# Performance work log

Measured on AMD Instinct MI355X. Metric: run time of the kernel, lower is better.

The kernel has to match this reference:

```python
import jax, jax.numpy as jnp
import numpy as np

N_NODES = 100000


def _gcn_layer(x, W, b, src, dst, ew):
    # support = x @ W  (dense transform first, standard GCN)
    support = x @ W  # [N, out]
    # sparse propagate: out[i] = sum_{e: dst[e]=i} ew[e] * support[src[e]]
    msgs = support[src] * ew[:, None]  # [E, out]
    out = jax.ops.segment_sum(msgs, dst, num_segments=N_NODES)
    return out + b


def setup_inputs() -> dict:
    key = jax.random.key(0)
    ks = jax.random.split(key, 7)
    nfeat, nhid, nclass, E = 512, 256, 40, 3200000
    x = jax.random.normal(ks[0], (N_NODES, nfeat), dtype=jnp.float32)
    edge_index = jax.random.randint(ks[1], (2, E), 0, N_NODES, dtype=jnp.int32)
    edge_weight = jax.random.uniform(ks[2], (E,), dtype=jnp.float32)
    W1 = jax.random.normal(ks[3], (nfeat, nhid), dtype=jnp.float32) / np.sqrt(nfeat)
    b1 = jnp.zeros((nhid,), dtype=jnp.float32)
    W2 = jax.random.normal(ks[4], (nhid, nclass), dtype=jnp.float32) / np.sqrt(nhid)
    b2 = jnp.zeros((nclass,), dtype=jnp.float32)
    return {"x": x, "edge_index": edge_index, "edge_weight": edge_weight,
            "W1": W1, "b1": b1, "W2": W2, "b2": b2}


def reference(x, edge_index, edge_weight, W1, b1, W2, b2):
    src, dst = edge_index[0], edge_index[1]
    h = _gcn_layer(x, W1, b1, src, dst, edge_weight)
    h = jax.nn.relu(h)  # with_relu=True; dropout skipped (eval mode)
    h = _gcn_layer(h, W2, b2, src, dst, edge_weight)
    return jax.nn.log_softmax(h, axis=1)
```

## Files before the change

kernel.cpp:

```cpp
#include <hip/hip_runtime.h>
#include <math.h>

#define N_NODES 100000
#define M_PAD 100096
#define NFEAT 512
#define NHID 256
#define NCLASS 40
#define SUP2_LD 48

#define NBKT 250
#define NPB 400
#define BINA_CHUNK 3072
#define BCAP 14336

#define GEMM1_TILES 782
#define GEMM1_BLOCKS 391

typedef __attribute__((ext_vector_type(8))) short bf16x8;
typedef __attribute__((ext_vector_type(4))) float f32x4;

__device__ __forceinline__ unsigned short f2bf(float f) {
    unsigned int u = __builtin_bit_cast(unsigned int, f);
    u += 0x7fffu + ((u >> 16) & 1u);
    return (unsigned short)(u >> 16);
}
__device__ __forceinline__ void bf2x2(unsigned int u, float& f0, float& f1) {
    f0 = __builtin_bit_cast(float, u << 16);
    f1 = __builtin_bit_cast(float, u & 0xffff0000u);
}
__device__ __forceinline__ void gload16(const void* g, void* l) {
    __builtin_amdgcn_global_load_lds(
        (const __attribute__((address_space(1))) unsigned int*)g,
        (__attribute__((address_space(3))) unsigned int*)l, 16, 0, 0);
}
template <int CODE>
__device__ __forceinline__ float swzx(float v) {
    return __builtin_bit_cast(float,
        __builtin_amdgcn_ds_swizzle(__builtin_bit_cast(int, v), CODE));
}

#define CVTW_BLOCKS 512

__global__ __launch_bounds__(256) void k_init(int* __restrict__ bcur,
                                              const float* __restrict__ W1,
                                              unsigned short* __restrict__ w1t,
                                              const float* __restrict__ W2,
                                              uint4* __restrict__ w2f) {
    int b = blockIdx.x;
    int t = threadIdx.x;
    if (b == 0) {
        if (t < NBKT) bcur[t] = t * BCAP;
    } else if (b <= CVTW_BLOCKS) {
        int idx = (b - 1) * 256 + t;
        int n = idx >> 9, k = idx & 511;
        w1t[idx] = f2bf(W1[(size_t)k * NHID + n]);
    } else {
        for (int idx = t; idx < 8 * 3 * 64; idx += 256) {
            int ks = idx / 192;
            int rem = idx - ks * 192;
            int n = rem >> 6;
            int l = rem & 63;
            int col = n * 16 + (l & 15);
            int kbase = ks * 32 + (l >> 4) * 8;
            unsigned short o[8];
#pragma unroll
            for (int j = 0; j < 8; ++j)
                o[j] = (col < NCLASS) ? f2bf(W2[(size_t)(kbase + j) * NCLASS + col]) : 0;
            w2f[idx] = *(const uint4*)o;
        }
    }
}

__device__ __forceinline__ void binA_body(char* smbase, int t, int cblk,
                                          const int* __restrict__ src,
                                          const int* __restrict__ dst,
                                          const float* __restrict__ ew,
                                          int* __restrict__ bcur,
                                          uint2* __restrict__ tmp, int E) {
    uint2* sorted = (uint2*)smbase;
    unsigned char* bkt8 = (unsigned char*)(smbase + 24576);
    int* cnt = (int*)(smbase + 27648);
    int* startv = cnt + 256;
    int* offv = startv + 256;
    int* gb = offv + 256;
    int c0 = cblk * BINA_CHUNK;
    int n = min(BINA_CHUNK, E - c0);
    cnt[t] = 0;
    __syncthreads();
    for (int j = t; j < n; j += 256) {
        atomicAdd(&cnt[(unsigned)dst[c0 + j] / NPB], 1);
    }
    __syncthreads();
    int v = cnt[t];
    startv[t] = v;
    __syncthreads();
    for (int o = 1; o < 256; o <<= 1) {
        int a = (t >= o) ? startv[t - o] : 0;
        __syncthreads();
        startv[t] += a;
        __syncthreads();
    }
    int ex = startv[t] - v;
    __syncthreads();
    startv[t] = ex;
    offv[t] = ex;
    if (t < NBKT) gb[t] = (v > 0) ? atomicAdd(&bcur[t], v) : 0;
    __syncthreads();
    for (int j = t; j < n; j += 256) {
        int d = dst[c0 + j];
        int b = (unsigned)d / NPB;
        int dl = d - b * NPB;
        int r = atomicAdd(&offv[b], 1);
        sorted[r] = make_uint2((unsigned)src[c0 + j] | ((unsigned)dl << 17),
                               __builtin_bit_cast(unsigned, ew[c0 + j]));
        bkt8[r] = (unsigned char)b;
    }
    __syncthreads();
    for (int j = t; j < n; j += 256) {
        int b = bkt8[j];
        tmp[gb[b] + (j - startv[b])] = sorted[j];
    }
}

__device__ __forceinline__ void gemm1_body(char* smem, int t, int mb,
                                           const float* __restrict__ x,
                                           const unsigned short* __restrict__ w1t,
                                           unsigned short* __restrict__ sup1) {
    const int w = t >> 6, lane = t & 63;
    const int m0 = mb * 128;
    const int wm = w >> 1, wn = w & 1;
    const int r15 = lane & 15, hi = lane >> 4;

    f32x4 acc[4][8];
#pragma unroll
    for (int i = 0; i < 4; ++i)
#pragma unroll
        for (int j = 0; j < 8; ++j) acc[i][j] = (f32x4){0.f, 0.f, 0.f, 0.f};

    const char* wsrc = (const char*)w1t;

#define STAGE1(kt, b)                                                                  \
    {                                                                                  \
        char* Ab = smem + (b) * 8192;                                                  \
        char* Bb = smem + 16384 + (b) * 16384;                                         \
        _Pragma("unroll") for (int i = 0; i < 2; ++i) {                                \
            int u = i * 256 + t;                                                       \
            int row = u >> 2, part = u & 3;                                            \
            int gr = m0 + row;                                                         \
            unsigned short ob[8];                                                      \
            if (gr < N_NODES) {                                                        \
                const float* sp = x + (size_t)gr * NFEAT + (kt) * 32 + part * 8;       \
                float4 v0 = *(const float4*)sp;                                        \
                float4 v1 = *(const float4*)(sp + 4);                                  \
                ob[0] = f2bf(v0.x); ob[1] = f2bf(v0.y);                                \
                ob[2] = f2bf(v0.z); ob[3] = f2bf(v0.w);                                \
                ob[4] = f2bf(v1.x); ob[5] = f2bf(v1.y);                                \
                ob[6] = f2bf(v1.z); ob[7] = f2bf(v1.w);                                \
            } else {                                                                   \
                _Pragma("unroll") for (int j = 0; j < 8; ++j) ob[j] = 0;               \
            }                                                                          \
            *(uint4*)(Ab + row * 64 + ((part ^ ((row >> 1) & 3)) << 4)) =              \
                *(const uint4*)ob;                                                     \
        }                                                                              \
        _Pragma("unroll") for (int i = 0; i < 4; ++i) {                                \
            int u = i * 256 + t;                                                       \
            int nrow = u >> 2, part = u & 3;                                           \
            int q = part ^ ((nrow >> 1) & 3);                                          \
            gload16(wsrc + (size_t)nrow * 1024 + (kt) * 64 + q * 16, Bb + u * 16);     \
        }                                                                              \
    }

    STAGE1(0, 0);
    for (int kt = 0; kt < 16; ++kt) {
        __syncthreads();
        if (kt < 15) STAGE1(kt + 1, (kt + 1) & 1);
        const char* Ab = smem + (kt & 1) * 8192;
        const char* Bb = smem + 16384 + (kt & 1) * 16384;
        bf16x8 a[4], bb[8];
#pragma unroll
        for (int i = 0; i < 4; ++i) {
            int r = wm * 64 + i * 16 + r15;
            a[i] = *(const bf16x8*)(Ab + r * 64 + ((hi ^ ((r >> 1) & 3)) << 4));
        }
#pragma unroll
        for (int j = 0; j < 8; ++j) {
            int n = wn * 128 + j * 16 + r15;
            bb[j] = *(const bf16x8*)(Bb + n * 64 + ((hi ^ ((n >> 1) & 3)) << 4));
        }
#pragma unroll
        for (int i = 0; i < 4; ++i)
#pragma unroll
            for (int j = 0; j < 8; ++j)
                acc[i][j] = __builtin_amdgcn_mfma_f32_16x16x32_bf16(a[i], bb[j], acc[i][j], 0, 0, 0);
    }
#undef STAGE1

#pragma unroll
    for (int i = 0; i < 4; ++i) {
        int rowb = m0 + wm * 64 + i * 16 + hi * 4;
#pragma unroll
        for (int j = 0; j < 8; ++j) {
            int col = wn * 128 + j * 16 + r15;
#pragma unroll
            for (int r = 0; r < 4; ++r)
                sup1[(size_t)(rowb + r) * NHID + col] = f2bf(acc[i][j][r]);
        }
    }
}

__global__ __launch_bounds__(256) void k_fat(const float* __restrict__ x,
                                             const unsigned short* __restrict__ w1t,
                                             unsigned short* __restrict__ sup1,
                                             const int* __restrict__ src,
                                             const int* __restrict__ dst,
                                             const float* __restrict__ ew,
                                             int* __restrict__ bcur,
                                             uint2* __restrict__ tmp, int E) {
    __shared__ __align__(16) char smem[49152];
    int b = blockIdx.x;
    int t = threadIdx.x;
    if (b < GEMM1_BLOCKS) {
        gemm1_body(smem, t, b, x, w1t, sup1);
        __syncthreads();
        gemm1_body(smem, t, b + GEMM1_BLOCKS, x, w1t, sup1);
    } else {
        binA_body(smem, t, b - GEMM1_BLOCKS, src, dst, ew, bcur, tmp, E);
    }
}

__global__ __launch_bounds__(256) void k_binB(const uint2* __restrict__ tmp,
                                              const int* __restrict__ bcur,
                                              int* __restrict__ rowptr,
                                              uint2* __restrict__ cedge) {
    __shared__ int sc[256];
    __shared__ int nc[NPB];
    __shared__ int st[NPB];
    int b = blockIdx.x, t = threadIdx.x;
    int c = (t < NBKT) ? (bcur[t] - t * BCAP) : 0;
    sc[t] = c;
    __syncthreads();
    for (int o = 1; o < 256; o <<= 1) {
        int a = (t >= o) ? sc[t - o] : 0;
        __syncthreads();
        sc[t] += a;
        __syncthreads();
    }
    int base = (b == 0) ? 0 : sc[b - 1];
    int mycnt = sc[b] - base;
    int total = sc[NBKT - 1];
    __syncthreads();
    for (int i = t; i < NPB; i += 256) nc[i] = 0;
    __syncthreads();
    const uint2* srcp = tmp + (size_t)b * BCAP;
    for (int j = t; j < mycnt; j += 256) atomicAdd(&nc[srcp[j].x >> 17], 1);
    __syncthreads();
    int v0 = nc[t];
    sc[t] = v0;
    __syncthreads();
    for (int o = 1; o < 256; o <<= 1) {
        int a = (t >= o) ? sc[t - o] : 0;
        __syncthreads();
        sc[t] += a;
        __syncthreads();
    }
    int tot0 = sc[255];
    st[t] = sc[t] - v0;
    __syncthreads();
    int v1 = (t < NPB - 256) ? nc[256 + t] : 0;
    sc[t] = v1;
    __syncthreads();
    for (int o = 1; o < 256; o <<= 1) {
        int a = (t >= o) ? sc[t - o] : 0;
        __syncthreads();
        sc[t] += a;
        __syncthreads();
    }
    if (t < NPB - 256) st[256 + t] = tot0 + sc[t] - v1;
    __syncthreads();
    int n0 = b * NPB;
    for (int i = t; i < NPB; i += 256) {
        int s = base + st[i];
        rowptr[n0 + i] = s;
        st[i] = s;
    }
    if (b == NBKT - 1 && t == 0) rowptr[N_NODES] = total;
    __syncthreads();
    for (int j = t; j < mycnt; j += 256) {
        uint2 e = srcp[j];
        int dl = e.x >> 17;
        int addr = atomicAdd(&st[dl], 1);
        cedge[addr] = make_uint2(e.x & 0x1FFFFu, e.y);
    }
}

__global__ __launch_bounds__(256) void k_prop1(const unsigned short* __restrict__ sup1,
                                               const int* __restrict__ rowptr,
                                               const uint2* __restrict__ cedge,
                                               const float* __restrict__ b1,
                                               unsigned short* __restrict__ h1) {
    int gid = blockIdx.x * blockDim.x + threadIdx.x;
    int wid = gid >> 6;
    int lane = gid & 63;
    if (wid >= N_NODES) return;
    int beg = rowptr[wid], end = rowptr[wid + 1];
    float a0 = 0.f, a1 = 0.f, a2 = 0.f, a3 = 0.f;
    int e = beg;
    for (; e + 7 < end; e += 8) {
        uint2 ed[8];
#pragma unroll
        for (int q = 0; q < 8; ++q) ed[q] = cedge[e + q];
        uint2 r[8];
#pragma unroll
        for (int q = 0; q < 8; ++q)
            r[q] = *(const uint2*)(sup1 + (size_t)ed[q].x * NHID + lane * 4);
#pragma unroll
        for (int q = 0; q < 8; ++q) {
            float wq = __builtin_bit_cast(float, ed[q].y);
            float f0, f1, f2, f3;
            bf2x2(r[q].x, f0, f1);
            bf2x2(r[q].y, f2, f3);
            a0 += wq * f0; a1 += wq * f1; a2 += wq * f2; a3 += wq * f3;
        }
    }
    for (; e < end; ++e) {
        uint2 ed = cedge[e];
        float wq = __builtin_bit_cast(float, ed.y);
        uint2 rv = *(const uint2*)(sup1 + (size_t)ed.x * NHID + lane * 4);
        float f0, f1, f2, f3;
        bf2x2(rv.x, f0, f1);
        bf2x2(rv.y, f2, f3);
        a0 += wq * f0; a1 += wq * f1; a2 += wq * f2; a3 += wq * f3;
    }
    float4 bv = *(const float4*)(b1 + lane * 4);
    a0 = fmaxf(a0 + bv.x, 0.f);
    a1 = fmaxf(a1 + bv.y, 0.f);
    a2 = fmaxf(a2 + bv.z, 0.f);
    a3 = fmaxf(a3 + bv.w, 0.f);
    unsigned short o[4] = {f2bf(a0), f2bf(a1), f2bf(a2), f2bf(a3)};
    *(uint2*)(h1 + (size_t)wid * NHID + lane * 4) = *(const uint2*)o;
}

__global__ __launch_bounds__(256) void k_gemm2(const unsigned short* __restrict__ h1,
                                               const uint4* __restrict__ w2f,
                                               unsigned short* __restrict__ sup2) {
    int t = threadIdx.x;
    int w = t >> 6, lane = t & 63;
    int m0 = (blockIdx.x * 4 + w) * 16;
    int r15 = lane & 15, hi = lane >> 4;

    bf16x8 bfrag[8][3];
#pragma unroll
    for (int ks = 0; ks < 8; ++ks)
#pragma unroll
        for (int n = 0; n < 3; ++n)
            bfrag[ks][n] = __builtin_bit_cast(bf16x8, w2f[(ks * 3 + n) * 64 + lane]);

    f32x4 acc[3];
#pragma unroll
    for (int n = 0; n < 3; ++n) acc[n] = (f32x4){0.f, 0.f, 0.f, 0.f};

    const unsigned short* arow = h1 + (size_t)(m0 + r15) * NHID + hi * 8;
#pragma unroll
    for (int ks = 0; ks < 8; ++ks) {
        bf16x8 a = *(const bf16x8*)(arow + ks * 32);
#pragma unroll
        for (int n = 0; n < 3; ++n)
            acc[n] = __builtin_amdgcn_mfma_f32_16x16x32_bf16(a, bfrag[ks][n], acc[n], 0, 0, 0);
    }
#pragma unroll
    for (int n = 0; n < 3; ++n) {
        int col = n * 16 + r15;
#pragma unroll
        for (int r = 0; r < 4; ++r) {
            int row = m0 + hi * 4 + r;
            sup2[(size_t)row * SUP2_LD + col] = f2bf(acc[n][r]);
        }
    }
}

__global__ __launch_bounds__(256) void k_prop2(const unsigned short* __restrict__ sup2,
                                               const int* __restrict__ rowptr,
                                               const uint2* __restrict__ cedge,
                                               const float* __restrict__ b2,
                                               float* __restrict__ out) {
    int gid = blockIdx.x * blockDim.x + threadIdx.x;
    int wv = gid >> 6;
    int lane = gid & 63;
    int grp = lane >> 4;
    int gl = lane & 15;
    int wid = wv * 4 + grp;
    if (wid >= N_NODES) return;
    int beg = rowptr[wid], end = rowptr[wid + 1];
    bool act = gl < 10;
    int c4 = gl * 4;
    float acc0 = 0.f, acc1 = 0.f, acc2 = 0.f, acc3 = 0.f;
    int e = beg;
    for (; e + 7 < end; e += 8) {
        uint2 ed[8];
#pragma unroll
        for (int q = 0; q < 8; ++q) ed[q] = cedge[e + q];
        uint2 u[8];
#pragma unroll
        for (int q = 0; q < 8; ++q)
            u[q] = act ? *(const uint2*)(sup2 + (size_t)ed[q].x * SUP2_LD + c4)
                       : make_uint2(0u, 0u);
#pragma unroll
        for (int q = 0; q < 8; ++q) {
            float wq = __builtin_bit_cast(float, ed[q].y);
            float f0, f1, f2, f3;
            bf2x2(u[q].x, f0, f1);
            bf2x2(u[q].y, f2, f3);
            acc0 += wq * f0; acc1 += wq * f1; acc2 += wq * f2; acc3 += wq * f3;
        }
    }
    for (; e < end; ++e) {
        uint2 eq = cedge[e];
        uint2 u = act ? *(const uint2*)(sup2 + (size_t)eq.x * SUP2_LD + c4)
                      : make_uint2(0u, 0u);
        float wq = __builtin_bit_cast(float, eq.y);
        float f0, f1, f2, f3;
        bf2x2(u.x, f0, f1);
        bf2x2(u.y, f2, f3);
        acc0 += wq * f0; acc1 += wq * f1; acc2 += wq * f2; acc3 += wq * f3;
    }
    float v0 = -INFINITY, v1 = -INFINITY, v2 = -INFINITY, v3 = -INFINITY;
    if (act) {
        float4 bb = *(const float4*)(b2 + c4);
        v0 = acc0 + bb.x;
        v1 = acc1 + bb.y;
        v2 = acc2 + bb.z;
        v3 = acc3 + bb.w;
    }
    float m = fmaxf(fmaxf(v0, v1), fmaxf(v2, v3));
    m = fmaxf(m, swzx<0x201F>(m));
    m = fmaxf(m, swzx<0x101F>(m));
    m = fmaxf(m, swzx<0x081F>(m));
    m = fmaxf(m, swzx<0x041F>(m));
    float s = act ? (expf(v0 - m) + expf(v1 - m) + expf(v2 - m) + expf(v3 - m)) : 0.f;
    s += swzx<0x201F>(s);
    s += swzx<0x101F>(s);
    s += swzx<0x081F>(s);
    s += swzx<0x041F>(s);
    if (act) {
        float ls = logf(s);
        float4 o = make_float4(v0 - m - ls, v1 - m - ls, v2 - m - ls, v3 - m - ls);
        *(float4*)(out + (size_t)wid * NCLASS + c4) = o;
    }
}


extern "C" void kernel_launch(void* const* d_in, const int* in_sizes, int n_in,
                              void* d_out, int out_size, void* d_ws, size_t ws_size,
                              hipStream_t stream) {
    const float* x = (const float*)d_in[0];
    const int* ei = (const int*)d_in[1];
    const float* ew = (const float*)d_in[2];
    const float* W1 = (const float*)d_in[3];
    const float* b1 = (const float*)d_in[4];
    const float* W2 = (const float*)d_in[5];
    const float* b2 = (const float*)d_in[6];
    float* out = (float*)d_out;

    int E = in_sizes[1] / 2;
    const int* src = ei;
    const int* dst = ei + E;

    char* w = (char*)d_ws;
    size_t off = 0;
    auto alloc = [&](size_t bytes) {
        void* p = w + off;
        off += (bytes + 255) & ~(size_t)255;
        return p;
    };
    unsigned short* w1t = (unsigned short*)alloc((size_t)NHID * NFEAT * 2);
    unsigned short* sup1 = (unsigned short*)alloc((size_t)M_PAD * NHID * 2);
    unsigned short* h1 = (unsigned short*)alloc((size_t)M_PAD * NHID * 2);
    uint2* cedge = (uint2*)alloc((size_t)E * 8);
    uint2* tmp = (uint2*)alloc((size_t)NBKT * BCAP * 8);
    unsigned short* sup2 = (unsigned short*)alloc((size_t)M_PAD * SUP2_LD * 2);
    int* rowptr = (int*)alloc((size_t)(N_NODES + 1) * 4);
    int* bcur = (int*)alloc((size_t)NBKT * 4);
    uint4* w2f = (uint4*)alloc((size_t)8 * 3 * 64 * 16);

    const int BINA_BLOCKS = (E + BINA_CHUNK - 1) / BINA_CHUNK;

    k_init<<<1 + CVTW_BLOCKS + 1, 256, 0, stream>>>(bcur, W1, w1t, W2, w2f);
    k_fat<<<GEMM1_BLOCKS + BINA_BLOCKS, 256, 0, stream>>>(x, w1t, sup1,
                                                          src, dst, ew, bcur, tmp, E);
    k_binB<<<NBKT, 256, 0, stream>>>(tmp, bcur, rowptr, cedge);
    k_prop1<<<(N_NODES + 3) / 4, 256, 0, stream>>>(sup1, rowptr, cedge, b1, h1);
    k_gemm2<<<M_PAD / 64, 256, 0, stream>>>(h1, w2f, sup2);
    k_prop2<<<(N_NODES / 4 + 3) / 4, 256, 0, stream>>>(sup2, rowptr, cedge, b2, out);
}
```

Before: 544.2 us.

## Prefetch GEMM1 A tiles into registers and give each block one tile

```diff
diff --git a/kernel.cpp b/kernel.cpp
--- a/kernel.cpp
+++ b/kernel.cpp
@@ -13,8 +13,7 @@
 #define BINA_CHUNK 3072
 #define BCAP 14336
 
-#define GEMM1_TILES 782
-#define GEMM1_BLOCKS 391
+#define GEMM1_BLOCKS (M_PAD / 128)
 
 typedef __attribute__((ext_vector_type(8))) short bf16x8;
 typedef __attribute__((ext_vector_type(4))) float f32x4;
@@ -139,29 +138,50 @@
 
     const char* wsrc = (const char*)w1t;
 
-#define STAGE1(kt, b)                                                                  \
+    float4 pa0, pa1, pa2, pa3;
+
+#define A_LOAD(kt)                                                                     \
+    {                                                                                  \
+        int u0 = t, row0 = u0 >> 2, part0 = u0 & 3;                                    \
+        int u1 = 256 + t, row1 = u1 >> 2, part1 = u1 & 3;                              \
+        int gr0 = m0 + row0, gr1 = m0 + row1;                                          \
+        if (gr0 < N_NODES) {                                                           \
+            const float* sp = x + (size_t)gr0 * NFEAT + (kt) * 32 + part0 * 8;         \
+            pa0 = *(const float4*)sp;                                                  \
+            pa1 = *(const float4*)(sp + 4);                                            \
+        } else {                                                                       \
+            pa0 = pa1 = make_float4(0.f, 0.f, 0.f, 0.f);                               \
+        }                                                                              \
+        if (gr1 < N_NODES) {                                                           \
+            const float* sp = x + (size_t)gr1 * NFEAT + (kt) * 32 + part1 * 8;         \
+            pa2 = *(const float4*)sp;                                                  \
+            pa3 = *(const float4*)(sp + 4);                                            \
+        } else {                                                                       \
+            pa2 = pa3 = make_float4(0.f, 0.f, 0.f, 0.f);                               \
+        }                                                                              \
+    }
+
+#define A_STORE(b)                                                                     \
     {                                                                                  \
         char* Ab = smem + (b) * 8192;                                                  \
+        int u0 = t, row0 = u0 >> 2, part0 = u0 & 3;                                    \
+        int u1 = 256 + t, row1 = u1 >> 2, part1 = u1 & 3;                              \
+        unsigned short ob[8];                                                          \
+        ob[0] = f2bf(pa0.x); ob[1] = f2bf(pa0.y); ob[2] = f2bf(pa0.z);                 \
+        ob[3] = f2bf(pa0.w); ob[4] = f2bf(pa1.x); ob[5] = f2bf(pa1.y);                 \
+        ob[6] = f2bf(pa1.z); ob[7] = f2bf(pa1.w);                                      \
+        *(uint4*)(Ab + row0 * 64 + ((part0 ^ ((row0 >> 1) & 3)) << 4)) =               \
+            *(const uint4*)ob;                                                         \
+        ob[0] = f2bf(pa2.x); ob[1] = f2bf(pa2.y); ob[2] = f2bf(pa2.z);                 \
+        ob[3] = f2bf(pa2.w); ob[4] = f2bf(pa3.x); ob[5] = f2bf(pa3.y);                 \
+        ob[6] = f2bf(pa3.z); ob[7] = f2bf(pa3.w);                                      \
+        *(uint4*)(Ab + row1 * 64 + ((part1 ^ ((row1 >> 1) & 3)) << 4)) =               \
+            *(const uint4*)ob;                                                         \
+    }
+
+#define B_STAGE(kt, b)                                                                 \
+    {                                                                                  \
         char* Bb = smem + 16384 + (b) * 16384;                                         \
-        _Pragma("unroll") for (int i = 0; i < 2; ++i) {                                \
-            int u = i * 256 + t;                                                       \
-            int row = u >> 2, part = u & 3;                                            \
-            int gr = m0 + row;                                                         \
-            unsigned short ob[8];                                                      \
-            if (gr < N_NODES) {                                                        \
-                const float* sp = x + (size_t)gr * NFEAT + (kt) * 32 + part * 8;       \
-                float4 v0 = *(const float4*)sp;                                        \
-                float4 v1 = *(const float4*)(sp + 4);                                  \
-                ob[0] = f2bf(v0.x); ob[1] = f2bf(v0.y);                                \
-                ob[2] = f2bf(v0.z); ob[3] = f2bf(v0.w);                                \
-                ob[4] = f2bf(v1.x); ob[5] = f2bf(v1.y);                                \
-                ob[6] = f2bf(v1.z); ob[7] = f2bf(v1.w);                                \
-            } else {                                                                   \
-                _Pragma("unroll") for (int j = 0; j < 8; ++j) ob[j] = 0;               \
-            }                                                                          \
-            *(uint4*)(Ab + row * 64 + ((part ^ ((row >> 1) & 3)) << 4)) =              \
-                *(const uint4*)ob;                                                     \
-        }                                                                              \
         _Pragma("unroll") for (int i = 0; i < 4; ++i) {                                \
             int u = i * 256 + t;                                                       \
             int nrow = u >> 2, part = u & 3;                                           \
@@ -170,10 +190,15 @@
         }                                                                              \
     }
 
-    STAGE1(0, 0);
+    A_LOAD(0);
+    A_STORE(0);
+    B_STAGE(0, 0);
     for (int kt = 0; kt < 16; ++kt) {
         __syncthreads();
-        if (kt < 15) STAGE1(kt + 1, (kt + 1) & 1);
+        if (kt < 15) {
+            A_LOAD(kt + 1);
+            B_STAGE(kt + 1, (kt + 1) & 1);
+        }
         const char* Ab = smem + (kt & 1) * 8192;
         const char* Bb = smem + 16384 + (kt & 1) * 16384;
         bf16x8 a[4], bb[8];
@@ -192,8 +217,11 @@
 #pragma unroll
             for (int j = 0; j < 8; ++j)
                 acc[i][j] = __builtin_amdgcn_mfma_f32_16x16x32_bf16(a[i], bb[j], acc[i][j], 0, 0, 0);
-    }
-#undef STAGE1
+        if (kt < 15) A_STORE((kt + 1) & 1);
+    }
+#undef A_LOAD
+#undef A_STORE
+#undef B_STAGE
 
 #pragma unroll
     for (int i = 0; i < 4; ++i) {
@@ -221,8 +249,6 @@
     int t = threadIdx.x;
     if (b < GEMM1_BLOCKS) {
         gemm1_body(smem, t, b, x, w1t, sup1);
-        __syncthreads();
-        gemm1_body(smem, t, b + GEMM1_BLOCKS, x, w1t, sup1);
     } else {
         binA_body(smem, t, b - GEMM1_BLOCKS, src, dst, ew, bcur, tmp, E);
     }
```

After: 478.5 us. 12.1% less time.
